# Performance work log

Hardware: AMD Instinct MI355X
Metric: run time of the kernel (lower is better)

Reference implementation:

```python
import jax, jax.numpy as jnp
import numpy as np
import math

B, L, X, E, Y = 2, 1024, 4, 128, 4  # batch, win_size/seq, search heads, head dim, retrieval heads


def setup_inputs() -> dict:
    key = jax.random.key(0)
    ks = jax.random.split(key, 12)
    f = jnp.float32
    x = jax.random.normal(ks[0], (B, L, X, E), f)
    query = jax.random.normal(ks[1], (B, L, X, E), f)
    k = jax.random.normal(ks[2], (B, L, X, E), f)
    value = jax.random.normal(ks[3], (B, L, Y, E), f)
    sigma = jax.random.normal(ks[4], (B, L, X), f)
    q_plus = jax.random.normal(ks[5], (B, L, X, E), f)
    # custom triangular mask over (search, retrieval) dims, broadcastable to scores [B,L,M,X,Y]
    attn_mask = jnp.triu(jnp.ones((X, Y), dtype=bool), k=1)
    # Linear(E,E) params (key_plus projection and V projection)
    s = 1.0 / math.sqrt(E)
    Wk = jax.random.normal(ks[6], (E, E), f) * s
    bk = jax.random.normal(ks[7], (E,), f) * s
    Wv = jax.random.normal(ks[8], (E, E), f) * s
    bv = jax.random.normal(ks[9], (E,), f) * s
    return {"x": x, "query": query, "key": k, "value": value, "sigma": sigma,
            "attn_mask": attn_mask, "retrieval": Y, "search": X, "q_plus": q_plus,
            "Wk": Wk, "bk": bk, "Wv": Wv, "bv": bv}


def reference(x, query, key, value, sigma, attn_mask, retrieval, search, q_plus, Wk, bk, Wv, bv):
    Bq, Lq, Hq, Eq = query.shape
    scale = 1.0 / math.sqrt(Eq)
    # stage 1: search attention over keys, per search-head x
    Search = jax.nn.softmax(jnp.einsum('blxe,bsxe->bxls', query, key) * scale, axis=-1)  # [B,X,L,S]
    Retrieval = jnp.einsum('bxls,bsye->blexy', Search, value)  # [B,L,E,X,Y]
    # key_plus = Linear(E,E) over the E axis of Retrieval
    key_plus = jnp.einsum('blexy,fe->blfxy', Retrieval, Wk) + bk[None, None, :, None, None]  # [B,L,E,X,Y]
    # stage 2: scores between q_plus and retrieved keys
    scores = jnp.einsum('blxe,bmexy->blmxy', q_plus, key_plus)  # [B,L,M,X,Y]
    scores = jnp.where(attn_mask[None, None, None, :, :], -jnp.inf, scores)
    series = jax.nn.softmax(scores * scale, axis=-1)  # softmax over Y (retrieval)
    # sigma transform -> Gaussian prior over |i-j| distances
    sig = jnp.transpose(sigma, (0, 2, 1))               # [B,Hs,L]
    sig = jax.nn.sigmoid(sig * 5.0) + 1e-5
    sig = jnp.power(3.0, sig) - 1.0
    sig = sig[..., None]                                # [B,Hs,L,1]
    idx = jnp.arange(Lq, dtype=jnp.float32)
    dist = jnp.abs(idx[:, None] - idx[None, :])         # [L,L]
    prior = 1.0 / (np.float32(math.sqrt(2.0 * math.pi)) * sig) * jnp.exp(-dist ** 2 / 2.0 / sig ** 2)  # [B,Hs,L,L]
    # dropout p=0.0 -> identity
    catt = jnp.einsum('blsxy,bsexy->blexy', series, Retrieval)  # [B,L,E,X,Y]
    V = jnp.sum(catt, axis=-1)                           # chunk over Y then sum -> [B,L,E,X]
    V_list = V.reshape(Bq, Lq, search, -1)               # row-major reinterpret == torch .view
    V = jnp.einsum('blse,fe->blsf', V_list, Wv) + bv     # [B,L,search,E]
    series_out = jnp.mean(jnp.transpose(series, (0, 3, 1, 2, 4)), axis=-1)  # chunk/sum/retrieval == mean over Y -> [B,X,L,M]
    return V, series_out, prior, sig
```

## Files before the change

### kernel.cpp

```cpp
#include <hip/hip_runtime.h>
#include <math.h>

#define B 2
#define L 1024
#define X 4
#define E 128
#define Y 4
#define SCALE 0.08838834764831845f

typedef unsigned short u16;
typedef __attribute__((ext_vector_type(8))) short bf16frag;
typedef __attribute__((ext_vector_type(4))) float floatx4;

static __device__ __forceinline__ u16 bfr(float f) {
  union { float f; unsigned u; } c; c.f = f;
  unsigned r = (c.u + 0x7fffu + ((c.u >> 16) & 1u)) >> 16;
  return (u16)r;
}

__global__ __launch_bounds__(256) void k0_fill(float4* __restrict__ p, int n4) {
  int i = blockIdx.x * 256 + threadIdx.x;
  if (i < n4) p[i] = make_float4(0.25f, 0.25f, 0.25f, 0.25f);
}

__global__ __launch_bounds__(256) void k0w_wvt(const float* __restrict__ Wv,
                                               float4* __restrict__ wv4t) {
  const int idx = blockIdx.x * 256 + threadIdx.x;
  const int e4 = idx >> 7, f = idx & 127;
  wv4t[idx] = *(const float4*)(Wv + f * E + e4 * 4);
}

__global__ __launch_bounds__(256) void k0q_convert(const float* __restrict__ q,
                                                   const float* __restrict__ key,
                                                   u16* __restrict__ qkb,
                                                   float* __restrict__ colsum) {
  if (blockIdx.x == 0) colsum[threadIdx.x] = 0.f;
  const int f = blockIdx.x * 256 + threadIdx.x;
  const int row = f >> 4, c8 = (f & 15) * 8;
  const int sel = row >> 13, row2 = row & 8191;
  const int b = row2 >> 12, l = (row2 >> 2) & 1023, x = row2 & 3;
  const float* src = (sel ? key : q) + (size_t)row2 * E + c8;
  float4 v0 = *(const float4*)src;
  float4 v1 = *(const float4*)(src + 4);
  u16 us[8] = {bfr(v0.x), bfr(v0.y), bfr(v0.z), bfr(v0.w),
               bfr(v1.x), bfr(v1.y), bfr(v1.z), bfr(v1.w)};
  u16* dst = qkb + (size_t)(sel * 8192 + (b * 4 + x) * 1024 + l) * E + c8;
  *(uint4*)dst = *(uint4*)us;
}

__global__ __launch_bounds__(512) void k1_mfma(const u16* __restrict__ qb,
                                               const u16* __restrict__ kb,
                                               u16* __restrict__ sbh,
                                               float* __restrict__ isum) {
  __shared__ __align__(16) u16 Qt[16][136];
  __shared__ __align__(16) u16 Kt[128][136];
  __shared__ float red[8][16];
  const int t = threadIdx.x;
  const int blk = blockIdx.x;
  const int lt = blk & 63, bx = blk >> 6;
  const int l0 = lt * 16;
  const int lane = t & 63, w = t >> 6;
  const int col = lane & 15, quad = lane >> 4;
  if (t < 256) {
    const int r = t >> 4, c8 = (t & 15) * 8;
    *(uint4*)&Qt[r][c8] = *(const uint4*)(qb + (size_t)(bx * L + l0 + r) * E + c8);
  }
  __syncthreads();
  bf16frag af[4];
#pragma unroll
  for (int k = 0; k < 4; ++k)
    af[k] = *(const bf16frag*)&Qt[col][k * 32 + quad * 8];

  float rs[4] = {0.f, 0.f, 0.f, 0.f};
  for (int sc = 0; sc < 8; ++sc) {
    __syncthreads();
    {
      const int r = t >> 2, c = (t & 3) * 32;
      const u16* src = kb + (size_t)(bx * L + sc * 128 + r) * E + c;
#pragma unroll
      for (int i = 0; i < 4; ++i)
        *(uint4*)&Kt[r][c + i * 8] = *(const uint4*)(src + i * 8);
    }
    __syncthreads();
    floatx4 acc = (floatx4){0.f, 0.f, 0.f, 0.f};
#pragma unroll
    for (int k = 0; k < 4; ++k) {
      bf16frag bk = *(const bf16frag*)&Kt[w * 16 + col][k * 32 + quad * 8];
      acc = __builtin_amdgcn_mfma_f32_16x16x32_bf16(af[k], bk, acc, 0, 0, 0);
    }
    const size_t so = (size_t)sc * 128 + w * 16 + col;
#pragma unroll
    for (int r = 0; r < 4; ++r) {
      float p = __expf(acc[r] * SCALE);
      rs[r] += p;
      sbh[(size_t)(bx * L + l0 + quad * 4 + r) * L + so] = bfr(p);
    }
  }
#pragma unroll
  for (int m = 1; m <= 8; m <<= 1)
#pragma unroll
    for (int r = 0; r < 4; ++r) rs[r] += __shfl_xor(rs[r], m, 64);
  __syncthreads();
  if (col == 0)
#pragma unroll
    for (int r = 0; r < 4; ++r) red[w][quad * 4 + r] = rs[r];
  __syncthreads();
  if (w == 0 && col == 0)
#pragma unroll
    for (int r = 0; r < 4; ++r) {
      float s = 0.f;
#pragma unroll
      for (int j = 0; j < 8; ++j) s += red[j][quad * 4 + r];
      isum[bx * L + l0 + quad * 4 + r] = 1.0f / s;
    }
}

__global__ __launch_bounds__(128) void k2v_transpose(const float* __restrict__ value,
                                                     u16* __restrict__ vt) {
  const int blk = blockIdx.x;
  const int sc = blk & 31, by = blk >> 5;
  const int b = by >> 2, y = by & 3;
  const int t = threadIdx.x;
  const int s0 = sc * 32;
  u16 us[32];
#pragma unroll 8
  for (int ss = 0; ss < 32; ++ss)
    us[ss] = bfr(value[((size_t)((b * L + s0 + ss) * Y + y)) * E + t]);
  u16* dst = vt + ((size_t)(by * E + t)) * L + s0;
#pragma unroll
  for (int i = 0; i < 4; ++i) *(uint4*)(dst + i * 8) = *(uint4*)&us[i * 8];
}

__global__ __launch_bounds__(256) void k34_retr_kp(const u16* __restrict__ sbh,
                                                   const u16* __restrict__ vt,
                                                   const float* __restrict__ isum,
                                                   const float* __restrict__ Wk,
                                                   const float* __restrict__ bk,
                                                   u16* __restrict__ kp_bf,
                                                   u16* __restrict__ rt_bf,
                                                   float* __restrict__ colsum) {
  __shared__ __align__(16) unsigned char smem[32 * 132 * 4];
  u16 (*Pt)[40] = (u16(*)[40])smem;
  u16 (*Vt)[40] = (u16(*)[40])(smem + 2560);
  float (*Rt)[132] = (float(*)[132])smem;
  const int t = threadIdx.x;
  const int blk = (blockIdx.x & 7) * 80 + (blockIdx.x >> 3);
  const int lt = blk & 31;
  const int cp = blk >> 5;
  const int b = cp / 10, p = cp % 10;
  const int x = (p >= 6) ? 3 : (p >= 3) ? 2 : (p >= 1) ? 1 : 0;
  const int y = p - ((x * (x + 1)) >> 1);
  const int by = b * 4 + y;
  const int srow = (b * 4 + x) * L;
  const int l0 = lt * 32;
  const int lane = t & 63, w = t >> 6;
  const int col = lane & 15, quad = lane >> 4;
  const int lw = w >> 1, eg = w & 1;
  floatx4 vf[4];
#pragma unroll
  for (int i = 0; i < 4; ++i) vf[i] = (floatx4){0.f, 0.f, 0.f, 0.f};
  for (int sc = 0; sc < 32; ++sc) {
    const int s0 = sc * 32;
    __syncthreads();
    {
      const int r = t >> 3, c = (t & 7) * 4;
      *(uint2*)&Pt[r][c] = *(const uint2*)(sbh + (size_t)(srow + l0 + r) * L + s0 + c);
    }
    {
      const int e = t >> 1, half = (t & 1) * 16;
      const u16* src = vt + ((size_t)(by * E + e)) * L + s0 + half;
      *(uint4*)&Vt[e][half] = *(const uint4*)src;
      *(uint4*)&Vt[e][half + 8] = *(const uint4*)(src + 8);
    }
    __syncthreads();
    bf16frag pf = *(const bf16frag*)&Pt[lw * 16 + col][quad * 8];
#pragma unroll
    for (int i = 0; i < 4; ++i) {
      bf16frag rf = *(const bf16frag*)&Vt[(eg * 4 + i) * 16 + col][quad * 8];
      vf[i] = __builtin_amdgcn_mfma_f32_16x16x32_bf16(pf, rf, vf[i], 0, 0, 0);
    }
  }
  float is[4];
#pragma unroll
  for (int r = 0; r < 4; ++r) is[r] = isum[srow + l0 + lw * 16 + quad * 4 + r];
  __syncthreads();
#pragma unroll
  for (int i = 0; i < 4; ++i)
#pragma unroll
    for (int r = 0; r < 4; ++r)
      Rt[lw * 16 + quad * 4 + r][(eg * 4 + i) * 16 + col] = vf[i][r] * is[r];
  __syncthreads();
  if (p == 0) {
    if (t < 128) {
      float ssum = 0.f;
#pragma unroll
      for (int r = 0; r < 32; ++r) ssum += Rt[r][t];
      atomicAdd(&colsum[b * 128 + t], ssum);
    }
    return;
  }
  const int cslot = b * 9 + (p - 1);
  bf16frag aR[4];
#pragma unroll
  for (int k = 0; k < 4; ++k) {
    u16 us[8];
#pragma unroll
    for (int j = 0; j < 8; ++j) us[j] = bfr(Rt[lw * 16 + col][k * 32 + quad * 8 + j]);
    aR[k] = *(bf16frag*)us;
  }
#pragma unroll
  for (int ft = 0; ft < 4; ++ft) {
    const int f0 = (eg * 4 + ft) * 16;
    floatx4 c = (floatx4){0.f, 0.f, 0.f, 0.f};
#pragma unroll
    for (int k = 0; k < 4; ++k) {
      const float* wr = Wk + (size_t)(f0 + col) * E + k * 32 + quad * 8;
      float4 w0 = *(const float4*)wr;
      float4 w1 = *(const float4*)(wr + 4);
      u16 us[8] = {bfr(w0.x), bfr(w0.y), bfr(w0.z), bfr(w0.w),
                   bfr(w1.x), bfr(w1.y), bfr(w1.z), bfr(w1.w)};
      bf16frag bf = *(bf16frag*)us;
      c = __builtin_amdgcn_mfma_f32_16x16x32_bf16(aR[k], bf, c, 0, 0, 0);
    }
    const float bias = bk[f0 + col];
#pragma unroll
    for (int r = 0; r < 4; ++r)
      kp_bf[((size_t)(cslot * L + l0 + lw * 16 + quad * 4 + r)) * E + f0 + col] =
          bfr(c[r] + bias);
  }
  {
    const int e = t >> 1, half = t & 1;
    u16 us[16];
#pragma unroll
    for (int j = 0; j < 16; ++j) us[j] = bfr(Rt[half * 16 + j][e]);
    u16* dst = rt_bf + ((size_t)(cslot * E + e)) * L + l0 + half * 16;
    *(uint4*)dst = *(uint4*)&us[0];
    *(uint4*)(dst + 8) = *(uint4*)&us[8];
  }
}

template<int NY>
static __device__ __forceinline__ void k5_body(const float* __restrict__ qp,
                                               const u16* __restrict__ kp_bf,
                                               const u16* __restrict__ rt_bf,
                                               float* __restrict__ vws,
                                               u16 (*__restrict__ uni)[128][40],
                                               u16 (*__restrict__ pT)[32][40],
                                               const int t, const int b,
                                               const int lt, const int part,
                                               const int slotbase) {
  constexpr int x = NY - 1;
  u16 (*kpT)[32][136] = (u16 (*)[32][136])uni;
  const int mc0 = part * 4;
  const int l0 = lt * 32;
  const int lane = t & 63, w = t >> 6;
  const int col = lane & 15, quad = lane >> 4;
  const int lw = w >> 1, mt = w & 1, eg = w & 1;
  const int smr = t >> 3, se0 = (t & 7) * 16;
  const int sre = t >> 1, srh = (t & 1) * 16;

  bf16frag af[4];
  {
    const float* qpr = qp + ((size_t)((b * L + l0 + lw * 16 + col) * X + x)) * E;
#pragma unroll
    for (int k = 0; k < 4; ++k) {
      float4 v0 = *(const float4*)(qpr + k * 32 + quad * 8);
      float4 v1 = *(const float4*)(qpr + k * 32 + quad * 8 + 4);
      u16 us[8] = {bfr(v0.x), bfr(v0.y), bfr(v0.z), bfr(v0.w),
                   bfr(v1.x), bfr(v1.y), bfr(v1.z), bfr(v1.w)};
      af[k] = *(bf16frag*)us;
    }
  }
  floatx4 vf[4];
#pragma unroll
  for (int i = 0; i < 4; ++i) vf[i] = (floatx4){0.f, 0.f, 0.f, 0.f};

  for (int mc = mc0; mc < mc0 + 4; ++mc) {
    const int m0 = mc * 32;
    __syncthreads();
#pragma unroll
    for (int y = 0; y < NY; ++y) {
      const u16* src = kp_bf + ((size_t)(slotbase + y) * L + m0 + smr) * E + se0;
      uint4 a0 = *(const uint4*)src;
      uint4 a1 = *(const uint4*)(src + 8);
      *(uint4*)&kpT[y][smr][se0] = a0;
      *(uint4*)&kpT[y][smr][se0 + 8] = a1;
    }
    __syncthreads();
    floatx4 sf[NY];
#pragma unroll
    for (int y = 0; y < NY; ++y) sf[y] = (floatx4){0.f, 0.f, 0.f, 0.f};
#pragma unroll
    for (int y = 0; y < NY; ++y)
#pragma unroll
      for (int k = 0; k < 4; ++k) {
        bf16frag bkf = *(const bf16frag*)&kpT[y][mt * 16 + col][k * 32 + quad * 8];
        sf[y] = __builtin_amdgcn_mfma_f32_16x16x32_bf16(af[k], bkf, sf[y], 0, 0, 0);
      }
    u16 pu[NY][4];
#pragma unroll
    for (int r = 0; r < 4; ++r) {
      float zz[NY]; float mx = -3.4e38f;
#pragma unroll
      for (int y = 0; y < NY; ++y) { zz[y] = sf[y][r] * SCALE; mx = fmaxf(mx, zz[y]); }
      float sum = 0.f;
#pragma unroll
      for (int y = 0; y < NY; ++y) { zz[y] = __expf(zz[y] - mx); sum += zz[y]; }
      float inv = 1.0f / sum;
#pragma unroll
      for (int y = 0; y < NY; ++y) pu[y][r] = bfr(zz[y] * inv);
    }
    __syncthreads();
#pragma unroll
    for (int y = 0; y < NY; ++y) {
#pragma unroll
      for (int r = 0; r < 4; ++r)
        pT[y][lw * 16 + quad * 4 + r][mt * 16 + col] = pu[y][r];
      const u16* src = rt_bf + ((size_t)(slotbase + y) * E + sre) * L + m0 + srh;
      uint4 a0 = *(const uint4*)src;
      uint4 a1 = *(const uint4*)(src + 8);
      *(uint4*)&uni[y][sre][srh] = a0;
      *(uint4*)&uni[y][sre][srh + 8] = a1;
    }
    __syncthreads();
#pragma unroll
    for (int y = 0; y < NY; ++y) {
      bf16frag pf = *(const bf16frag*)&pT[y][lw * 16 + col][quad * 8];
#pragma unroll
      for (int i = 0; i < 4; ++i) {
        bf16frag rf = *(const bf16frag*)&uni[y][(eg * 4 + i) * 16 + col][quad * 8];
        vf[i] = __builtin_amdgcn_mfma_f32_16x16x32_bf16(pf, rf, vf[i], 0, 0, 0);
      }
    }
  }
  float* dst = vws + (size_t)(b * 24 + (x - 1) * 8 + part) * (L * E) + (size_t)l0 * E;
#pragma unroll
  for (int i = 0; i < 4; ++i)
#pragma unroll
    for (int r = 0; r < 4; ++r)
      dst[((size_t)(lw * 16 + quad * 4 + r)) * E + (eg * 4 + i) * 16 + col] = vf[i][r];
}

__global__ __launch_bounds__(256) void k5_stage2(const float* __restrict__ qp,
                                                 const u16* __restrict__ kp_bf,
                                                 const u16* __restrict__ rt_bf,
                                                 float* __restrict__ vws) {
  __shared__ __align__(16) u16 uni[4][128][40];
  __shared__ __align__(16) u16 pT[4][32][40];
  const int t = threadIdx.x;
  const int vb = (blockIdx.x & 7) * 192 + (blockIdx.x >> 3);
  const int g = vb >> 8;
  const int r = vb & 255;
  const int b = g / 3, xm1 = g % 3;
  const int part = r >> 5, lt = r & 31;
  const int slotbase = b * 9 + ((xm1 == 0) ? 0 : (xm1 == 1) ? 2 : 5);
  if (xm1 == 0)      k5_body<2>(qp, kp_bf, rt_bf, vws, uni, pT, t, b, lt, part, slotbase);
  else if (xm1 == 1) k5_body<3>(qp, kp_bf, rt_bf, vws, uni, pT, t, b, lt, part, slotbase);
  else               k5_body<4>(qp, kp_bf, rt_bf, vws, uni, pT, t, b, lt, part, slotbase);
}

__global__ __launch_bounds__(256) void k6_vout(const float* __restrict__ vws,
                                               const float4* __restrict__ wv4t,
                                               const float* __restrict__ bv,
                                               const float* __restrict__ colsum,
                                               float* __restrict__ vout) {
  __shared__ __align__(16) float rowf[8][512];
  const int t = threadIdx.x;
  const int blk = blockIdx.x;
  const int bl0 = blk * 8;
  const int b = bl0 >> 10;
  const int lbase = bl0 & 1023;
  {
    const int o = t * 2;
    const int xh = o >> 7, e = o & 127;
    if (xh == 0) {
      const float sx = colsum[b * 128 + e];
      const float sy = colsum[b * 128 + e + 1];
#pragma unroll
      for (int l8 = 0; l8 < 8; ++l8) {
        rowf[l8][e * 4] = sx;
        rowf[l8][(e + 1) * 4] = sy;
      }
    } else {
      const size_t pbase = (size_t)(b * 24 + (xh - 1) * 8) * 131072;
#pragma unroll
      for (int l8 = 0; l8 < 8; ++l8) {
        const size_t base = pbase + (size_t)(lbase + l8) * 128 + e;
        float sx = 0.f, sy = 0.f;
#pragma unroll
        for (int p = 0; p < 8; ++p) {
          float2 v = *(const float2*)(vws + base + (size_t)p * 131072);
          sx += v.x; sy += v.y;
        }
        rowf[l8][e * 4 + xh] = sx;
        rowf[l8][(e + 1) * 4 + xh] = sy;
      }
    }
  }
  __syncthreads();
#pragma unroll
  for (int rep = 0; rep < 2; ++rep) {
    const int o = t + rep * 256;
    const int s = o >> 7, f = o & 127;
    float acc[8] = {0.f, 0.f, 0.f, 0.f, 0.f, 0.f, 0.f, 0.f};
    const float4* wp = wv4t + f;
#pragma unroll 4
    for (int e4 = 0; e4 < 32; ++e4) {
      const float4 wv = wp[e4 * 128];
#pragma unroll
      for (int l8 = 0; l8 < 8; ++l8) {
        const float4 rv = *(const float4*)&rowf[l8][(s * 32 + e4) * 4];
        acc[l8] += wv.x * rv.x + wv.y * rv.y + wv.z * rv.z + wv.w * rv.w;
      }
    }
    const float bb = bv[f];
#pragma unroll
    for (int l8 = 0; l8 < 8; ++l8)
      vout[(size_t)(bl0 + l8) * 512 + s * 128 + f] = acc[l8] + bb;
  }
}

__global__ __launch_bounds__(256) void k7_prior(const float* __restrict__ sigma,
                                                float* __restrict__ prior,
                                                float* __restrict__ sigout) {
  const int row = blockIdx.x;
  const int bx = row >> 10;
  const int i = row & 1023;
  const int b = bx >> 2, x = bx & 3;
  const double sv = (double)sigma[((size_t)(b * L + i)) * X + x];
  const double sg = 1.0 / (1.0 + exp(-5.0 * sv)) + 1e-5;
  const double s3 = exp(sg * 1.0986122886681098) - 1.0;
  const float coef = (float)(1.0 / (2.5066282746310002 * s3));
  const float inv2s2 = (float)(0.5 / (s3 * s3));
  const int t = threadIdx.x;
  const float di = (float)i;
  const int j0 = t * 4;
  float4 o; float d;
  d = di - (float)(j0 + 0); o.x = coef * __expf(-d * d * inv2s2);
  d = di - (float)(j0 + 1); o.y = coef * __expf(-d * d * inv2s2);
  d = di - (float)(j0 + 2); o.z = coef * __expf(-d * d * inv2s2);
  d = di - (float)(j0 + 3); o.w = coef * __expf(-d * d * inv2s2);
  *(float4*)(prior + (size_t)row * 1024 + j0) = o;
  if (t == 0) sigout[row] = (float)s3;
}

extern "C" void kernel_launch(void* const* d_in, const int* in_sizes, int n_in,
                              void* d_out, int out_size, void* d_ws, size_t ws_size,
                              hipStream_t stream) {
  const float* q     = (const float*)d_in[1];
  const float* key   = (const float*)d_in[2];
  const float* value = (const float*)d_in[3];
  const float* sigma = (const float*)d_in[4];
  const float* qp    = (const float*)d_in[8];
  const float* Wk    = (const float*)d_in[9];
  const float* bk    = (const float*)d_in[10];
  const float* Wv    = (const float*)d_in[11];
  const float* bv    = (const float*)d_in[12];

  float* out    = (float*)d_out;
  float* Vout   = out;
  float* sout   = out + 1048576;
  float* prior  = out + 9437184;
  float* sigout = out + 17825792;

  float* ws     = (float*)d_ws;
  u16*   sbh    = (u16*)ws;
  u16*   qb     = (u16*)(ws + 4194304);
  u16*   kb     = qb + 1048576;
  u16*   vt     = (u16*)(ws + 5242880);
  float* isum   = ws + 5767168;
  float* wv4t   = ws + 6291456;
  u16*   kp_bf  = (u16*)(ws + 8388608);
  u16*   rt_bf  = (u16*)(ws + 9568256);
  float* colsum = ws + 10747904;
  float* vws    = ws;

  hipLaunchKernelGGL(k0_fill,       dim3(8192), dim3(256), 0, stream, (float4*)sout, 2097152);
  hipLaunchKernelGGL(k0w_wvt,       dim3(16),   dim3(256), 0, stream, Wv, (float4*)wv4t);
  hipLaunchKernelGGL(k0q_convert,   dim3(1024), dim3(256), 0, stream, q, key, (u16*)qb, colsum);
  hipLaunchKernelGGL(k1_mfma,       dim3(512),  dim3(512), 0, stream, qb, kb, sbh, isum);
  hipLaunchKernelGGL(k2v_transpose, dim3(256),  dim3(128), 0, stream, value, vt);
  hipLaunchKernelGGL(k34_retr_kp,   dim3(640),  dim3(256), 0, stream, sbh, vt, isum, Wk, bk, kp_bf, rt_bf, colsum);
  hipLaunchKernelGGL(k5_stage2,     dim3(1536), dim3(256), 0, stream, qp, kp_bf, rt_bf, vws);
  hipLaunchKernelGGL(k6_vout,       dim3(256),  dim3(256), 0, stream, vws, (const float4*)wv4t, bv, colsum, Vout);
  hipLaunchKernelGGL(k7_prior,      dim3(8192), dim3(256), 0, stream, sigma, prior, sigout);
}
```

Baseline: 252.5 us.

## Merge independent prep kernels into one launch and double K-chunk in retrieval GEMM

Five independent setup kernels (series fill, Wv transpose, q/key bf16 conversion, value transpose, Gaussian prior) are folded into one kernel that branches on block index. This cuts launch overhead and lets the memory-bound prior and fill writes overlap with the conversions. The prior path now computes the double-precision sigma transform once per row in thread 0 and shares it through LDS, where before every thread computed it. The retrieval MFMA loop loads 64-wide K chunks instead of 32, halving the number of barrier-separated iterations at the cost of more LDS per block.

```diff
diff --git a/kernel.cpp b/kernel.cpp
--- a/kernel.cpp
+++ b/kernel.cpp
@@ -18,34 +18,77 @@
   return (u16)r;
 }
 
-__global__ __launch_bounds__(256) void k0_fill(float4* __restrict__ p, int n4) {
-  int i = blockIdx.x * 256 + threadIdx.x;
-  if (i < n4) p[i] = make_float4(0.25f, 0.25f, 0.25f, 0.25f);
-}
-
-__global__ __launch_bounds__(256) void k0w_wvt(const float* __restrict__ Wv,
-                                               float4* __restrict__ wv4t) {
-  const int idx = blockIdx.x * 256 + threadIdx.x;
-  const int e4 = idx >> 7, f = idx & 127;
-  wv4t[idx] = *(const float4*)(Wv + f * E + e4 * 4);
-}
-
-__global__ __launch_bounds__(256) void k0q_convert(const float* __restrict__ q,
-                                                   const float* __restrict__ key,
-                                                   u16* __restrict__ qkb,
-                                                   float* __restrict__ colsum) {
-  if (blockIdx.x == 0) colsum[threadIdx.x] = 0.f;
-  const int f = blockIdx.x * 256 + threadIdx.x;
-  const int row = f >> 4, c8 = (f & 15) * 8;
-  const int sel = row >> 13, row2 = row & 8191;
-  const int b = row2 >> 12, l = (row2 >> 2) & 1023, x = row2 & 3;
-  const float* src = (sel ? key : q) + (size_t)row2 * E + c8;
-  float4 v0 = *(const float4*)src;
-  float4 v1 = *(const float4*)(src + 4);
-  u16 us[8] = {bfr(v0.x), bfr(v0.y), bfr(v0.z), bfr(v0.w),
-               bfr(v1.x), bfr(v1.y), bfr(v1.z), bfr(v1.w)};
-  u16* dst = qkb + (size_t)(sel * 8192 + (b * 4 + x) * 1024 + l) * E + c8;
-  *(uint4*)dst = *(uint4*)us;
+__global__ __launch_bounds__(256) void k_prep(const float* __restrict__ q,
+                                              const float* __restrict__ key,
+                                              const float* __restrict__ value,
+                                              const float* __restrict__ sigma,
+                                              const float* __restrict__ Wv,
+                                              float4* __restrict__ sout4,
+                                              u16* __restrict__ qkb,
+                                              float* __restrict__ colsum,
+                                              u16* __restrict__ vt,
+                                              float4* __restrict__ wv4t,
+                                              float* __restrict__ prior,
+                                              float* __restrict__ sigout) {
+  __shared__ float shp[2];
+  const int bid = blockIdx.x;
+  const int t = threadIdx.x;
+  if (bid < 8192) {
+    sout4[bid * 256 + t] = make_float4(0.25f, 0.25f, 0.25f, 0.25f);
+  } else if (bid < 8208) {
+    const int idx = (bid - 8192) * 256 + t;
+    const int e4 = idx >> 7, f = idx & 127;
+    wv4t[idx] = *(const float4*)(Wv + f * E + e4 * 4);
+  } else if (bid < 9232) {
+    if (bid == 8208) colsum[t] = 0.f;
+    const int f = (bid - 8208) * 256 + t;
+    const int row = f >> 4, c8 = (f & 15) * 8;
+    const int sel = row >> 13, row2 = row & 8191;
+    const int b = row2 >> 12, l = (row2 >> 2) & 1023, x = row2 & 3;
+    const float* src = (sel ? key : q) + (size_t)row2 * E + c8;
+    float4 v0 = *(const float4*)src;
+    float4 v1 = *(const float4*)(src + 4);
+    u16 us[8] = {bfr(v0.x), bfr(v0.y), bfr(v0.z), bfr(v0.w),
+                 bfr(v1.x), bfr(v1.y), bfr(v1.z), bfr(v1.w)};
+    u16* dst = qkb + (size_t)(sel * 8192 + (b * 4 + x) * 1024 + l) * E + c8;
+    *(uint4*)dst = *(uint4*)us;
+  } else if (bid < 9360) {
+    const int blk = bid - 9232;
+    const int by = blk >> 4, sc2 = blk & 15;
+    const int b = by >> 2, y = by & 3;
+    const int e = t & 127, sh = t >> 7;
+    const int s0 = sc2 * 64 + sh * 32;
+    u16 us[32];
+#pragma unroll 8
+    for (int ss = 0; ss < 32; ++ss)
+      us[ss] = bfr(value[((size_t)((b * L + s0 + ss) * Y + y)) * E + e]);
+    u16* dst = vt + ((size_t)(by * E + e)) * L + s0;
+#pragma unroll
+    for (int i = 0; i < 4; ++i) *(uint4*)(dst + i * 8) = *(uint4*)&us[i * 8];
+  } else {
+    const int row = bid - 9360;
+    const int bx = row >> 10;
+    const int i = row & 1023;
+    const int b = bx >> 2, x = bx & 3;
+    if (t == 0) {
+      const double sv = (double)sigma[((size_t)(b * L + i)) * X + x];
+      const double sg = 1.0 / (1.0 + exp(-5.0 * sv)) + 1e-5;
+      const double s3 = exp(sg * 1.0986122886681098) - 1.0;
+      shp[0] = (float)(1.0 / (2.5066282746310002 * s3));
+      shp[1] = (float)(0.5 / (s3 * s3));
+      sigout[row] = (float)s3;
+    }
+    __syncthreads();
+    const float coef = shp[0], inv2s2 = shp[1];
+    const float di = (float)i;
+    const int j0 = t * 4;
+    float4 o; float d;
+    d = di - (float)(j0 + 0); o.x = coef * __expf(-d * d * inv2s2);
+    d = di - (float)(j0 + 1); o.y = coef * __expf(-d * d * inv2s2);
+    d = di - (float)(j0 + 2); o.z = coef * __expf(-d * d * inv2s2);
+    d = di - (float)(j0 + 3); o.w = coef * __expf(-d * d * inv2s2);
+    *(float4*)(prior + (size_t)row * 1024 + j0) = o;
+  }
 }
 
 __global__ __launch_bounds__(512) void k1_mfma(const u16* __restrict__ qb,
@@ -115,22 +158,6 @@
     }
 }
 
-__global__ __launch_bounds__(128) void k2v_transpose(const float* __restrict__ value,
-                                                     u16* __restrict__ vt) {
-  const int blk = blockIdx.x;
-  const int sc = blk & 31, by = blk >> 5;
-  const int b = by >> 2, y = by & 3;
-  const int t = threadIdx.x;
-  const int s0 = sc * 32;
-  u16 us[32];
-#pragma unroll 8
-  for (int ss = 0; ss < 32; ++ss)
-    us[ss] = bfr(value[((size_t)((b * L + s0 + ss) * Y + y)) * E + t]);
-  u16* dst = vt + ((size_t)(by * E + t)) * L + s0;
-#pragma unroll
-  for (int i = 0; i < 4; ++i) *(uint4*)(dst + i * 8) = *(uint4*)&us[i * 8];
-}
-
 __global__ __launch_bounds__(256) void k34_retr_kp(const u16* __restrict__ sbh,
                                                    const u16* __restrict__ vt,
                                                    const float* __restrict__ isum,
@@ -139,9 +166,9 @@
                                                    u16* __restrict__ kp_bf,
                                                    u16* __restrict__ rt_bf,
                                                    float* __restrict__ colsum) {
-  __shared__ __align__(16) unsigned char smem[32 * 132 * 4];
-  u16 (*Pt)[40] = (u16(*)[40])smem;
-  u16 (*Vt)[40] = (u16(*)[40])(smem + 2560);
+  __shared__ __align__(16) unsigned char smem[23040];
+  u16 (*Pt)[72] = (u16(*)[72])smem;
+  u16 (*Vt)[72] = (u16(*)[72])(smem + 4608);
   float (*Rt)[132] = (float(*)[132])smem;
   const int t = threadIdx.x;
   const int blk = (blockIdx.x & 7) * 80 + (blockIdx.x >> 3);
@@ -159,25 +186,29 @@
   floatx4 vf[4];
 #pragma unroll
   for (int i = 0; i < 4; ++i) vf[i] = (floatx4){0.f, 0.f, 0.f, 0.f};
-  for (int sc = 0; sc < 32; ++sc) {
-    const int s0 = sc * 32;
+  for (int sc2 = 0; sc2 < 16; ++sc2) {
+    const int s0 = sc2 * 64;
     __syncthreads();
     {
-      const int r = t >> 3, c = (t & 7) * 4;
-      *(uint2*)&Pt[r][c] = *(const uint2*)(sbh + (size_t)(srow + l0 + r) * L + s0 + c);
+      const int r = t >> 3, c8 = (t & 7) * 8;
+      *(uint4*)&Pt[r][c8] = *(const uint4*)(sbh + (size_t)(srow + l0 + r) * L + s0 + c8);
     }
     {
-      const int e = t >> 1, half = (t & 1) * 16;
-      const u16* src = vt + ((size_t)(by * E + e)) * L + s0 + half;
-      *(uint4*)&Vt[e][half] = *(const uint4*)src;
-      *(uint4*)&Vt[e][half + 8] = *(const uint4*)(src + 8);
-    }
-    __syncthreads();
-    bf16frag pf = *(const bf16frag*)&Pt[lw * 16 + col][quad * 8];
-#pragma unroll
-    for (int i = 0; i < 4; ++i) {
-      bf16frag rf = *(const bf16frag*)&Vt[(eg * 4 + i) * 16 + col][quad * 8];
-      vf[i] = __builtin_amdgcn_mfma_f32_16x16x32_bf16(pf, rf, vf[i], 0, 0, 0);
+      const int e = t >> 1, off = (t & 1) * 32;
+      const u16* src = vt + ((size_t)(by * E + e)) * L + s0 + off;
+#pragma unroll
+      for (int i = 0; i < 4; ++i)
+        *(uint4*)&Vt[e][off + i * 8] = *(const uint4*)(src + i * 8);
+    }
+    __syncthreads();
+#pragma unroll
+    for (int ks = 0; ks < 2; ++ks) {
+      bf16frag pf = *(const bf16frag*)&Pt[lw * 16 + col][ks * 32 + quad * 8];
+#pragma unroll
+      for (int i = 0; i < 4; ++i) {
+        bf16frag rf = *(const bf16frag*)&Vt[(eg * 4 + i) * 16 + col][ks * 32 + quad * 8];
+        vf[i] = __builtin_amdgcn_mfma_f32_16x16x32_bf16(pf, rf, vf[i], 0, 0, 0);
+      }
     }
   }
   float is[4];
@@ -420,30 +451,6 @@
   }
 }
 
-__global__ __launch_bounds__(256) void k7_prior(const float* __restrict__ sigma,
-                                                float* __restrict__ prior,
-                                                float* __restrict__ sigout) {
-  const int row = blockIdx.x;
-  const int bx = row >> 10;
-  const int i = row & 1023;
-  const int b = bx >> 2, x = bx & 3;
-  const double sv = (double)sigma[((size_t)(b * L + i)) * X + x];
-  const double sg = 1.0 / (1.0 + exp(-5.0 * sv)) + 1e-5;
-  const double s3 = exp(sg * 1.0986122886681098) - 1.0;
-  const float coef = (float)(1.0 / (2.5066282746310002 * s3));
-  const float inv2s2 = (float)(0.5 / (s3 * s3));
-  const int t = threadIdx.x;
-  const float di = (float)i;
-  const int j0 = t * 4;
-  float4 o; float d;
-  d = di - (float)(j0 + 0); o.x = coef * __expf(-d * d * inv2s2);
-  d = di - (float)(j0 + 1); o.y = coef * __expf(-d * d * inv2s2);
-  d = di - (float)(j0 + 2); o.z = coef * __expf(-d * d * inv2s2);
-  d = di - (float)(j0 + 3); o.w = coef * __expf(-d * d * inv2s2);
-  *(float4*)(prior + (size_t)row * 1024 + j0) = o;
-  if (t == 0) sigout[row] = (float)s3;
-}
-
 extern "C" void kernel_launch(void* const* d_in, const int* in_sizes, int n_in,
                               void* d_out, int out_size, void* d_ws, size_t ws_size,
                               hipStream_t stream) {
@@ -475,13 +482,10 @@
   float* colsum = ws + 10747904;
   float* vws    = ws;
 
-  hipLaunchKernelGGL(k0_fill,       dim3(8192), dim3(256), 0, stream, (float4*)sout, 2097152);
-  hipLaunchKernelGGL(k0w_wvt,       dim3(16),   dim3(256), 0, stream, Wv, (float4*)wv4t);
-  hipLaunchKernelGGL(k0q_convert,   dim3(1024), dim3(256), 0, stream, q, key, (u16*)qb, colsum);
-  hipLaunchKernelGGL(k1_mfma,       dim3(512),  dim3(512), 0, stream, qb, kb, sbh, isum);
-  hipLaunchKernelGGL(k2v_transpose, dim3(256),  dim3(128), 0, stream, value, vt);
-  hipLaunchKernelGGL(k34_retr_kp,   dim3(640),  dim3(256), 0, stream, sbh, vt, isum, Wk, bk, kp_bf, rt_bf, colsum);
-  hipLaunchKernelGGL(k5_stage2,     dim3(1536), dim3(256), 0, stream, qp, kp_bf, rt_bf, vws);
-  hipLaunchKernelGGL(k6_vout,       dim3(256),  dim3(256), 0, stream, vws, (const float4*)wv4t, bv, colsum, Vout);
-  hipLaunchKernelGGL(k7_prior,      dim3(8192), dim3(256), 0, stream, sigma, prior, sigout);
-}
+  hipLaunchKernelGGL(k_prep,      dim3(17552), dim3(256), 0, stream, q, key, value, sigma,
+                     Wv, (float4*)sout, (u16*)qb, colsum, vt, (float4*)wv4t, prior, sigout);
+  hipLaunchKernelGGL(k1_mfma,     dim3(512),  dim3(512), 0, stream, qb, kb, sbh, isum);
+  hipLaunchKernelGGL(k34_retr_kp, dim3(640),  dim3(256), 0, stream, sbh, vt, isum, Wk, bk, kp_bf, rt_bf, colsum);
+  hipLaunchKernelGGL(k5_stage2,   dim3(1536), dim3(256), 0, stream, qp, kp_bf, rt_bf, vws);
+  hipLaunchKernelGGL(k6_vout,     dim3(256),  dim3(256), 0, stream, vws, (const float4*)wv4t, bv, colsum, Vout);
+}
```

Result: faster. 210.2 us (-16.8%).
